# Kernel optimization log

Measured on AMD Instinct MI355X. Metric: run time of the kernel, lower is better.

Reference implementation:

```python
import jax, jax.numpy as jnp
import numpy as np

N, E, F_IN, F_E = 50000, 800000, 128, 16
R, H, C = 4, 4, 32            # num_relations, heads, out_channels
HC = H * C                     # 128
NEG_SLOPE = 0.2                # PyG RGATConv default negative_slope
EPS = 1e-16                    # PyG softmax epsilon


def rgat_conv(x, src, dst, edge_type, edge_attr, w, q, k, e, le, b, concat):
    """Faithful PyG RGATConv (additive-self-attention, across-relation, dim=1, aggr=add).
    x: [N,F]; w: [R,F,H*C]; q,k,e: [H*C,H]; le: [F_e,H*C]; b: bias."""
    n = x.shape[0]
    xw = jnp.einsum('nf,rfo->rno', x, w)              # [R,N,H*C] per-relation projections
    x_i = xw[edge_type, dst]                          # [E,H*C] target-node proj per edge
    x_j = xw[edge_type, src]                          # [E,H*C] source-node proj per edge
    qi = x_i @ q                                      # [E,H]
    kj = x_j @ k + (edge_attr @ le) @ e               # [E,H] (edge features folded into keys)
    alpha = jax.nn.leaky_relu(qi + kj, NEG_SLOPE)     # [E,H]
    # softmax over incoming edges of each destination node (across relations)
    amax = jax.ops.segment_max(alpha, dst, num_segments=n)
    ex = jnp.exp(alpha - amax[dst])
    denom = jax.ops.segment_sum(ex, dst, num_segments=n)
    alpha = ex / (denom[dst] + EPS)
    msg = alpha[:, :, None] * x_j.reshape(-1, H, C)   # [E,H,C]
    out = jax.ops.segment_sum(msg, dst, num_segments=n)  # [N,H,C] sum aggregation
    out = out.reshape(n, H * C) if concat else out.mean(axis=1)
    return out + b


def setup_inputs() -> dict:
    key = jax.random.key(0)
    ks = jax.random.split(key, 18)
    p = 0.05
    inp = {
        'x': jax.random.normal(ks[0], (N, F_IN), dtype=jnp.float32),
        'edge_index': jax.random.randint(ks[1], (2, E), 0, N, dtype=jnp.int64)
            if jax.config.jax_enable_x64 else jax.random.randint(ks[1], (2, E), 0, N).astype(jnp.int32),
        'edge_attr': jax.random.normal(ks[2], (E, F_E), dtype=jnp.float32),
        'edge_type': jax.random.randint(ks[3], (E,), 0, R).astype(jnp.int32),
        # conv1 params (in=F_IN, concat=True -> bias of size H*C)
        'w1': jax.random.normal(ks[4], (R, F_IN, HC), dtype=jnp.float32) * p,
        'q1': jax.random.normal(ks[5], (HC, H), dtype=jnp.float32) * p,
        'k1': jax.random.normal(ks[6], (HC, H), dtype=jnp.float32) * p,
        'e1': jax.random.normal(ks[7], (HC, H), dtype=jnp.float32) * p,
        'le1': jax.random.normal(ks[8], (F_E, HC), dtype=jnp.float32) * p,
        'b1': jnp.zeros((HC,), dtype=jnp.float32),
        # conv3 params (in=H*C=128, concat=False -> bias of size C)
        'w3': jax.random.normal(ks[9], (R, HC, HC), dtype=jnp.float32) * p,
        'q3': jax.random.normal(ks[10], (HC, H), dtype=jnp.float32) * p,
        'k3': jax.random.normal(ks[11], (HC, H), dtype=jnp.float32) * p,
        'e3': jax.random.normal(ks[12], (HC, H), dtype=jnp.float32) * p,
        'le3': jax.random.normal(ks[13], (F_E, HC), dtype=jnp.float32) * p,
        'b3': jnp.zeros((C,), dtype=jnp.float32),
    }
    return inp


def reference(x, edge_index, edge_attr, edge_type,
              w1, q1, k1, e1, le1, b1,
              w3, q3, k3, e3, le3, b3):
    src, dst = edge_index[0], edge_index[1]
    h = jax.nn.relu(rgat_conv(x, src, dst, edge_type, edge_attr,
                              w1, q1, k1, e1, le1, b1, concat=True))
    out = rgat_conv(h, src, dst, edge_type, edge_attr,
                    w3, q3, k3, e3, le3, b3, concat=False)
    return out
```

## Files before the change

kernel.cpp:

```cpp
#include <hip/hip_runtime.h>


#define NEG_SLOPE 0.2f
#define SOFT_EPS 1e-16f

typedef __attribute__((ext_vector_type(8))) short bf16x8;
typedef __attribute__((ext_vector_type(4))) float f32x4;
typedef __attribute__((ext_vector_type(4))) unsigned short u16x4;
typedef __attribute__((ext_vector_type(4))) _Float16 half4;
typedef __attribute__((ext_vector_type(8))) _Float16 half8;

__device__ __forceinline__ void bf16split(float f, unsigned short& h, unsigned short& l) {
  unsigned u = __float_as_uint(f);
  unsigned r = u + 0x7FFFu + ((u >> 16) & 1u);
  h = (unsigned short)(r >> 16);
  float fh = __uint_as_float(((unsigned)h) << 16);
  float d = f - fh;
  unsigned u2 = __float_as_uint(d);
  unsigned r2 = u2 + 0x7FFFu + ((u2 >> 16) & 1u);
  l = (unsigned short)(r2 >> 16);
}

__global__ void lee_kernel(const float* __restrict__ le1, const float* __restrict__ e1,
                           const float* __restrict__ le3, const float* __restrict__ e3,
                           float* __restrict__ lee) {
  int t = threadIdx.x;
  const float* le = (t < 64) ? le1 : le3;
  const float* ee = (t < 64) ? e1 : e3;
  int u = t & 63, f = u >> 2, h = u & 3;
  float acc = 0.f;
  for (int o = 0; o < 128; ++o) acc += le[f * 128 + o] * ee[o * 4 + h];
  lee[t] = acc;
}

__global__ __launch_bounds__(256) void wqk_kernel(
    const float* __restrict__ w1, const float* __restrict__ q1, const float* __restrict__ k1,
    const float* __restrict__ w3, const float* __restrict__ q3, const float* __restrict__ k3,
    float* __restrict__ wqk) {
  int idx = blockIdx.x * 256 + threadIdx.x;
  int L = idx >> 12, rem = idx & 4095;
  int r = rem >> 10, rem2 = rem & 1023, f = rem2 >> 3, j = rem2 & 7;
  const float* w = L ? w3 : w1;
  const float* qk = (j < 4) ? (L ? q3 : q1) : (L ? k3 : k1);
  int h = j & 3;
  const float* wrow = w + ((size_t)r * 128 + f) * 128;
  float acc = 0.f;
  for (int o = 0; o < 128; ++o) acc += wrow[o] * qk[o * 4 + h];
  wqk[idx] = acc;
}

__global__ __launch_bounds__(256) void hist_kernel(const int* __restrict__ dst,
                                                   int* __restrict__ deg, int E) {
  int e = blockIdx.x * 256 + threadIdx.x;
  if (e < E) atomicAdd(&deg[dst[e]], 1);
}

__global__ __launch_bounds__(256) void scanA_kernel(const int* __restrict__ deg,
                                                    int* __restrict__ bsum, int N) {
  int b = blockIdx.x, t = threadIdx.x;
  int base = b * 1024 + t * 4;
  int s = 0;
#pragma unroll
  for (int j = 0; j < 4; ++j) {
    int i = base + j;
    if (i < N) s += deg[i];
  }
#pragma unroll
  for (int o = 1; o < 64; o <<= 1) s += __shfl_xor(s, o);
  __shared__ int wsum[4];
  if ((t & 63) == 0) wsum[t >> 6] = s;
  __syncthreads();
  if (t == 0) bsum[b] = wsum[0] + wsum[1] + wsum[2] + wsum[3];
}

__global__ __launch_bounds__(256) void scanB_kernel(const int* __restrict__ bsum,
                                                    int* __restrict__ boff,
                                                    int* __restrict__ row_start,
                                                    int nb, int N) {
  int t = threadIdx.x;
  int v = (t < nb) ? bsum[t] : 0;
  int inc = v;
#pragma unroll
  for (int o = 1; o < 64; o <<= 1) {
    int u = __shfl_up(inc, o);
    if ((t & 63) >= o) inc += u;
  }
  __shared__ int wt[4];
  if ((t & 63) == 63) wt[t >> 6] = inc;
  __syncthreads();
  int add = 0;
  for (int wv = 0; wv < (t >> 6); ++wv) add += wt[wv];
  inc += add;
  if (t < nb) boff[t] = inc - v;
  if (t == 255) row_start[N] = inc;
}

__global__ __launch_bounds__(256) void scanC_kernel(const int* __restrict__ deg,
                                                    const int* __restrict__ boff,
                                                    int* __restrict__ row_start,
                                                    int* __restrict__ cursor, int N) {
  int b = blockIdx.x, t = threadIdx.x;
  int base = b * 1024 + t * 4;
  int d[4];
  int s = 0;
#pragma unroll
  for (int j = 0; j < 4; ++j) {
    int i = base + j;
    d[j] = (i < N) ? deg[i] : 0;
    s += d[j];
  }
  int inc = s;
#pragma unroll
  for (int o = 1; o < 64; o <<= 1) {
    int u = __shfl_up(inc, o);
    if ((t & 63) >= o) inc += u;
  }
  __shared__ int wt[4];
  if ((t & 63) == 63) wt[t >> 6] = inc;
  __syncthreads();
  int add = boff[b];
  for (int wv = 0; wv < (t >> 6); ++wv) add += wt[wv];
  int off = add + inc - s;
#pragma unroll
  for (int j = 0; j < 4; ++j) {
    int i = base + j;
    if (i < N) {
      row_start[i] = off;
      cursor[i] = off;
      off += d[j];
    }
  }
}

__global__ __launch_bounds__(256) void scatter_kernel(
    const int* __restrict__ src, const int* __restrict__ dst, const int* __restrict__ et,
    int* __restrict__ cursor, int4* __restrict__ es, int E) {
  int e = blockIdx.x * 256 + threadIdx.x;
  if (e >= E) return;
  int d = dst[e];
  int pos = atomicAdd(&cursor[d], 1);
  es[pos] = make_int4(src[e], d, et[e], e);
}

__global__ __launch_bounds__(256) void ek2_kernel(
    const int4* __restrict__ es, const float* __restrict__ ea,
    const float* __restrict__ lee, float* __restrict__ eks1,
    float* __restrict__ eks3, int E) {
  __shared__ float sl[128];
  if (threadIdx.x < 128) sl[threadIdx.x] = lee[threadIdx.x];
  __syncthreads();
  int i = blockIdx.x * 256 + threadIdx.x;
  if (i >= E) return;
  int eid = es[i].w;
  const float4* a4 = (const float4*)(ea + (size_t)eid * 16);
  float a1[4] = {0, 0, 0, 0}, a3[4] = {0, 0, 0, 0};
#pragma unroll
  for (int ii = 0; ii < 4; ++ii) {
    float4 v = a4[ii];
    int f = ii * 4;
#pragma unroll
    for (int h = 0; h < 4; ++h) {
      a1[h] += v.x * sl[f * 4 + h] + v.y * sl[(f + 1) * 4 + h] +
               v.z * sl[(f + 2) * 4 + h] + v.w * sl[(f + 3) * 4 + h];
      a3[h] += v.x * sl[64 + f * 4 + h] + v.y * sl[64 + (f + 1) * 4 + h] +
               v.z * sl[64 + (f + 2) * 4 + h] + v.w * sl[64 + (f + 3) * 4 + h];
    }
  }
  *(float4*)(eks1 + (size_t)i * 4) = make_float4(a1[0], a1[1], a1[2], a1[3]);
  *(float4*)(eks3 + (size_t)i * 4) = make_float4(a3[0], a3[1], a3[2], a3[3]);
}

__global__ __launch_bounds__(256) void convx_kernel(const float* __restrict__ in,
                                                    unsigned short* __restrict__ hi,
                                                    unsigned short* __restrict__ lo,
                                                    int total8) {
  int i = blockIdx.x * 256 + threadIdx.x;
  if (i >= total8) return;
  const float4* p = (const float4*)in + (size_t)i * 2;
  float4 a = p[0], b = p[1];
  float v[8] = {a.x, a.y, a.z, a.w, b.x, b.y, b.z, b.w};
  bf16x8 hv, lv;
#pragma unroll
  for (int j = 0; j < 8; ++j) {
    unsigned short h, l;
    bf16split(v[j], h, l);
    hv[j] = (short)h; lv[j] = (short)l;
  }
  *(bf16x8*)(hi + (size_t)i * 8) = hv;
  *(bf16x8*)(lo + (size_t)i * 8) = lv;
}

__global__ void convw_kernel(const float* __restrict__ w,
                             unsigned short* __restrict__ hiT,
                             unsigned short* __restrict__ loT) {
  int f = blockIdx.x, r = blockIdx.y, o = threadIdx.x;
  float v = w[((size_t)r * 128 + f) * 128 + o];
  unsigned short h, l;
  bf16split(v, h, l);
  hiT[((size_t)r * 128 + o) * 128 + f] = h;
  loT[((size_t)r * 128 + o) * 128 + f] = l;
}

__global__ __launch_bounds__(256) void proj_mfma_kernel(
    const unsigned short* __restrict__ xhi, const unsigned short* __restrict__ xlo,
    const unsigned short* __restrict__ whiT, const unsigned short* __restrict__ wloT,
    _Float16* __restrict__ xwh, int N) {
  __shared__ bf16x8 wl_h[2048];
  __shared__ bf16x8 wl_l[2048];
  int r = blockIdx.x;
  int nb = blockIdx.y * 128;
  int t = threadIdx.x;
  const unsigned short* wh = whiT + (size_t)r * (128 * 128);
  const unsigned short* wl = wloT + (size_t)r * (128 * 128);

#pragma unroll
  for (int j = 0; j < 8; ++j) {
    int i = j * 256 + t;
    int c = i & 15, q = (i >> 4) & 3, kc = (i >> 6) & 3, ot = i >> 8;
    int srco = (ot * 16 + c) * 128 + kc * 32 + q * 8;
    wl_h[i] = *(const bf16x8*)(wh + srco);
    wl_l[i] = *(const bf16x8*)(wl + srco);
  }
  __syncthreads();

  int wv = t >> 6;
  int lane = t & 63;
  int c = lane & 15, q = lane >> 4;
  int nodebase = nb + wv * 32;
  int n0 = nodebase + c;
  int n1 = nodebase + 16 + c;
  int n0c = n0 < N ? n0 : N - 1;
  int n1c = n1 < N ? n1 : N - 1;

  f32x4 acc[8][2];
#pragma unroll
  for (int ot = 0; ot < 8; ++ot)
#pragma unroll
    for (int nt = 0; nt < 2; ++nt) acc[ot][nt] = (f32x4){0.f, 0.f, 0.f, 0.f};

  bf16x8 xb[2][4];
  {
    int k0 = q * 8;
    xb[0][0] = *(const bf16x8*)(xhi + (size_t)n0c * 128 + k0);
    xb[0][1] = *(const bf16x8*)(xlo + (size_t)n0c * 128 + k0);
    xb[0][2] = *(const bf16x8*)(xhi + (size_t)n1c * 128 + k0);
    xb[0][3] = *(const bf16x8*)(xlo + (size_t)n1c * 128 + k0);
  }
#pragma unroll
  for (int kc = 0; kc < 4; ++kc) {
    if (kc < 3) {
      int k0 = (kc + 1) * 32 + q * 8;
      xb[(kc + 1) & 1][0] = *(const bf16x8*)(xhi + (size_t)n0c * 128 + k0);
      xb[(kc + 1) & 1][1] = *(const bf16x8*)(xlo + (size_t)n0c * 128 + k0);
      xb[(kc + 1) & 1][2] = *(const bf16x8*)(xhi + (size_t)n1c * 128 + k0);
      xb[(kc + 1) & 1][3] = *(const bf16x8*)(xlo + (size_t)n1c * 128 + k0);
    }
    bf16x8 b0h = xb[kc & 1][0], b0l = xb[kc & 1][1];
    bf16x8 b1h = xb[kc & 1][2], b1l = xb[kc & 1][3];
#pragma unroll
    for (int ot = 0; ot < 8; ++ot) {
      int fi = ((ot * 4 + kc) * 4 + q) * 16 + c;
      bf16x8 ah = wl_h[fi];
      bf16x8 al = wl_l[fi];
      acc[ot][0] = __builtin_amdgcn_mfma_f32_16x16x32_bf16(ah, b0h, acc[ot][0], 0, 0, 0);
      acc[ot][0] = __builtin_amdgcn_mfma_f32_16x16x32_bf16(ah, b0l, acc[ot][0], 0, 0, 0);
      acc[ot][0] = __builtin_amdgcn_mfma_f32_16x16x32_bf16(al, b0h, acc[ot][0], 0, 0, 0);
      acc[ot][1] = __builtin_amdgcn_mfma_f32_16x16x32_bf16(ah, b1h, acc[ot][1], 0, 0, 0);
      acc[ot][1] = __builtin_amdgcn_mfma_f32_16x16x32_bf16(ah, b1l, acc[ot][1], 0, 0, 0);
      acc[ot][1] = __builtin_amdgcn_mfma_f32_16x16x32_bf16(al, b1h, acc[ot][1], 0, 0, 0);
    }
  }

#pragma unroll
  for (int nt = 0; nt < 2; ++nt) {
    int n = nodebase + nt * 16 + c;
    if (n < N) {
      _Float16* basep = xwh + ((size_t)r * N + n) * 128 + q * 4;
#pragma unroll
      for (int ot = 0; ot < 8; ++ot) {
        f32x4 a = acc[ot][nt];
        half4 hv;
        hv[0] = (_Float16)a.x; hv[1] = (_Float16)a.y;
        hv[2] = (_Float16)a.z; hv[3] = (_Float16)a.w;
        *(half4*)(basep + ot * 16) = hv;
      }
    }
  }
}

__global__ __launch_bounds__(256) void qkx_kernel(
    const float* __restrict__ xin, const float* __restrict__ wqk,
    float* __restrict__ qn, float* __restrict__ kn, int N) {
  __shared__ float sx[64 * 132];
  __shared__ float swqk[4 * 1032];
  int nb = blockIdx.x * 64;
  int t = threadIdx.x;
#pragma unroll
  for (int j = 0; j < 16; ++j) {
    int i = j * 256 + t;
    swqk[(i >> 10) * 1032 + (i & 1023)] = wqk[i];
  }
#pragma unroll
  for (int j = 0; j < 8; ++j) {
    int i = j * 256 + t;
    int n = nb + (i >> 5); if (n >= N) n = N - 1;
    ((float4*)sx)[(i >> 5) * 33 + (i & 31)] =
        ((const float4*)(xin + (size_t)n * 128))[i & 31];
  }
  __syncthreads();
  int rl = t >> 2, r = t & 3;
  float aq0 = 0, aq1 = 0, aq2 = 0, aq3 = 0;
  float ak0 = 0, ak1 = 0, ak2 = 0, ak3 = 0;
  const float* xr = sx + rl * 132;
  const float* wb = swqk + r * 1032;
  for (int f = 0; f < 128; ++f) {
    float xv = xr[f];
    float4 qw = *(const float4*)(wb + f * 8);
    float4 kw = *(const float4*)(wb + f * 8 + 4);
    aq0 += xv * qw.x; aq1 += xv * qw.y; aq2 += xv * qw.z; aq3 += xv * qw.w;
    ak0 += xv * kw.x; ak1 += xv * kw.y; ak2 += xv * kw.z; ak3 += xv * kw.w;
  }
  int n = nb + rl;
  if (n < N) {
    *(float4*)(qn + ((size_t)r * N + n) * 4) = make_float4(aq0, aq1, aq2, aq3);
    *(float4*)(kn + ((size_t)r * N + n) * 4) = make_float4(ak0, ak1, ak2, ak3);
  }
}

__device__ __forceinline__ float4 edge_alpha(const int4* __restrict__ es,
                                             const float* __restrict__ qn,
                                             const float* __restrict__ kn,
                                             const float* __restrict__ eks,
                                             int i, int d, int N) {
  int4 v = es[i];
  float4 kv = *(const float4*)(kn + (v.z * N + v.x) * 4);
  float4 ev = ((const float4*)eks)[i];
  float4 q4 = *(const float4*)(qn + (v.z * N + d) * 4);
  float4 a = make_float4(q4.x + kv.x + ev.x, q4.y + kv.y + ev.y,
                         q4.z + kv.z + ev.z, q4.w + kv.w + ev.w);
  a.x = a.x > 0.f ? a.x : NEG_SLOPE * a.x;
  a.y = a.y > 0.f ? a.y : NEG_SLOPE * a.y;
  a.z = a.z > 0.f ? a.z : NEG_SLOPE * a.z;
  a.w = a.w > 0.f ? a.w : NEG_SLOPE * a.w;
  return a;
}

__global__ __launch_bounds__(256) void agg_kernel(
    const int4* __restrict__ es, const int* __restrict__ row_start,
    const float* __restrict__ qn, const float* __restrict__ kn,
    const float* __restrict__ eks, float* __restrict__ alpha_s,
    const _Float16* __restrict__ xwh, const float* __restrict__ bias,
    float* __restrict__ out, unsigned short* __restrict__ xhi,
    unsigned short* __restrict__ xlo, int N, int concat) {
  int d = blockIdx.x * 16 + (threadIdx.x >> 4);
  if (d >= N) return;
  int ql = threadIdx.x & 15;
  int rs = row_start[d], re = row_start[d + 1];
  int deg = re - rs;
  bool fast = (deg <= 64);

  float4 m = make_float4(-1e30f, -1e30f, -1e30f, -1e30f);
  float4 ar0 = m, ar1 = m, ar2 = m, ar3 = m;
  if (fast) {
#define SWEEPA(IT, AR)                                              \
    if (IT * 16 + ql < deg) {                                       \
      float4 a = edge_alpha(es, qn, kn, eks, rs + IT * 16 + ql, d, N); \
      AR = a;                                                       \
      m.x = fmaxf(m.x, a.x); m.y = fmaxf(m.y, a.y);                 \
      m.z = fmaxf(m.z, a.z); m.w = fmaxf(m.w, a.w);                 \
    }
    SWEEPA(0, ar0)
    SWEEPA(1, ar1)
    SWEEPA(2, ar2)
    SWEEPA(3, ar3)
#undef SWEEPA
  } else {
    for (int i = rs + ql; i < re; i += 16) {
      float4 a = edge_alpha(es, qn, kn, eks, i, d, N);
      ((float4*)alpha_s)[i] = a;
      m.x = fmaxf(m.x, a.x); m.y = fmaxf(m.y, a.y);
      m.z = fmaxf(m.z, a.z); m.w = fmaxf(m.w, a.w);
    }
  }
#pragma unroll
  for (int o = 1; o < 16; o <<= 1) {
    m.x = fmaxf(m.x, __shfl_xor(m.x, o));
    m.y = fmaxf(m.y, __shfl_xor(m.y, o));
    m.z = fmaxf(m.z, __shfl_xor(m.z, o));
    m.w = fmaxf(m.w, __shfl_xor(m.w, o));
  }

  float4 s = make_float4(0.f, 0.f, 0.f, 0.f);
  if (fast) {
#define SWEEPB(IT, AR)                                                       \
    if (IT * 16 + ql < deg) {                                                \
      float4 e4 = make_float4(__expf(AR.x - m.x), __expf(AR.y - m.y),        \
                              __expf(AR.z - m.z), __expf(AR.w - m.w));       \
      ((float4*)alpha_s)[rs + IT * 16 + ql] = e4;                            \
      s.x += e4.x; s.y += e4.y; s.z += e4.z; s.w += e4.w;                    \
    }
    SWEEPB(0, ar0)
    SWEEPB(1, ar1)
    SWEEPB(2, ar2)
    SWEEPB(3, ar3)
#undef SWEEPB
  } else {
    for (int i = rs + ql; i < re; i += 16) {
      float4 a = ((const float4*)alpha_s)[i];
      float4 e4 = make_float4(__expf(a.x - m.x), __expf(a.y - m.y),
                              __expf(a.z - m.z), __expf(a.w - m.w));
      ((float4*)alpha_s)[i] = e4;
      s.x += e4.x; s.y += e4.y; s.z += e4.z; s.w += e4.w;
    }
  }
#pragma unroll
  for (int o = 1; o < 16; o <<= 1) {
    s.x += __shfl_xor(s.x, o); s.y += __shfl_xor(s.y, o);
    s.z += __shfl_xor(s.z, o); s.w += __shfl_xor(s.w, o);
  }

  int h = ql >> 2;
  float smh = (h == 0) ? s.x : (h == 1) ? s.y : (h == 2) ? s.z : s.w;
  float rden = 1.f / (smh + SOFT_EPS);

  float acc[8];
#pragma unroll
  for (int j = 0; j < 8; ++j) acc[j] = 0.f;
  int e = rs;
  for (; e + 2 <= re; e += 2) {
    int4 a0 = es[e];
    int4 a1 = es[e + 1];
    float w0 = alpha_s[e * 4 + h];
    float w1 = alpha_s[(e + 1) * 4 + h];
    half8 x0 = *(const half8*)(xwh + (a0.z * N + a0.x) * 128 + ql * 8);
    half8 x1 = *(const half8*)(xwh + (a1.z * N + a1.x) * 128 + ql * 8);
#pragma unroll
    for (int j = 0; j < 8; ++j) {
      acc[j] = fmaf((float)x0[j], w0, acc[j]);
      acc[j] = fmaf((float)x1[j], w1, acc[j]);
    }
  }
  if (e < re) {
    int4 a0 = es[e];
    float w0 = alpha_s[e * 4 + h];
    half8 x0 = *(const half8*)(xwh + (a0.z * N + a0.x) * 128 + ql * 8);
#pragma unroll
    for (int j = 0; j < 8; ++j) acc[j] = fmaf((float)x0[j], w0, acc[j]);
  }
#pragma unroll
  for (int j = 0; j < 8; ++j) acc[j] *= rden;

  if (concat) {
    float4 b0 = ((const float4*)bias)[ql * 2];
    float4 b1 = ((const float4*)bias)[ql * 2 + 1];
    float v[8] = {acc[0] + b0.x, acc[1] + b0.y, acc[2] + b0.z, acc[3] + b0.w,
                  acc[4] + b1.x, acc[5] + b1.y, acc[6] + b1.z, acc[7] + b1.w};
    u16x4 hv0, lv0, hv1, lv1;
#pragma unroll
    for (int j = 0; j < 8; ++j) {
      v[j] = v[j] > 0.f ? v[j] : 0.f;
      unsigned short hh, ll;
      bf16split(v[j], hh, ll);
      if (j < 4) { hv0[j] = hh; lv0[j] = ll; }
      else { hv1[j - 4] = hh; lv1[j - 4] = ll; }
    }
    float* orow = out + (size_t)d * 128 + ql * 8;
    *(float4*)orow = make_float4(v[0], v[1], v[2], v[3]);
    *(float4*)(orow + 4) = make_float4(v[4], v[5], v[6], v[7]);
    *(u16x4*)(xhi + (size_t)d * 128 + ql * 8) = hv0;
    *(u16x4*)(xhi + (size_t)d * 128 + ql * 8 + 4) = hv1;
    *(u16x4*)(xlo + (size_t)d * 128 + ql * 8) = lv0;
    *(u16x4*)(xlo + (size_t)d * 128 + ql * 8 + 4) = lv1;
  } else {
#pragma unroll
    for (int j = 0; j < 8; ++j) {
      acc[j] += __shfl_xor(acc[j], 4);
      acc[j] += __shfl_xor(acc[j], 8);
    }
    if (ql < 4) {
      float4 b0 = ((const float4*)bias)[ql * 2];
      float4 b1 = ((const float4*)bias)[ql * 2 + 1];
      float* orow = out + (size_t)d * 32 + ql * 8;
      *(float4*)orow = make_float4(0.25f * acc[0] + b0.x, 0.25f * acc[1] + b0.y,
                                   0.25f * acc[2] + b0.z, 0.25f * acc[3] + b0.w);
      *(float4*)(orow + 4) = make_float4(0.25f * acc[4] + b1.x, 0.25f * acc[5] + b1.y,
                                         0.25f * acc[6] + b1.z, 0.25f * acc[7] + b1.w);
    }
  }
}

extern "C" void kernel_launch(void* const* d_in, const int* in_sizes, int n_in,
                              void* d_out, int out_size, void* d_ws, size_t ws_size,
                              hipStream_t stream) {
  const float* x   = (const float*)d_in[0];
  const int*   ei  = (const int*)d_in[1];
  const float* ea  = (const float*)d_in[2];
  const int*   etp = (const int*)d_in[3];
  const float* w1  = (const float*)d_in[4];
  const float* q1  = (const float*)d_in[5];
  const float* k1  = (const float*)d_in[6];
  const float* e1  = (const float*)d_in[7];
  const float* le1 = (const float*)d_in[8];
  const float* b1  = (const float*)d_in[9];
  const float* w3  = (const float*)d_in[10];
  const float* q3  = (const float*)d_in[11];
  const float* k3  = (const float*)d_in[12];
  const float* e3  = (const float*)d_in[13];
  const float* le3 = (const float*)d_in[14];
  const float* b3  = (const float*)d_in[15];
  const int N = in_sizes[0] / 128;
  const int E = in_sizes[3];
  const int* srcp = ei;
  const int* dstp = ei + E;

  float* ws   = (float*)d_ws;
  _Float16* xwh = (_Float16*)ws;
  float* qn   = ws + (size_t)2 * N * 128;
  float* kn   = qn + (size_t)4 * N * 4;
  float* eks1 = kn + (size_t)4 * N * 4;
  float* eks3 = eks1 + (size_t)E * 4;
  float* alph = eks3 + (size_t)E * 4;
  float* hbuf = alph + (size_t)E * 4;
  float* leeb = hbuf + (size_t)N * 128;
  float* wqkb = leeb + 128;
  int* deg      = (int*)(wqkb + 8192);
  int* rowst    = deg + N;
  int* cursor   = rowst + N + 1;
  int* bsum     = cursor + N;
  int* boff     = bsum + 256;
  uintptr_t pe = (uintptr_t)(boff + 256);
  pe = (pe + 15) & ~(uintptr_t)15;
  int4* es      = (int4*)pe;
  uintptr_t pa = (uintptr_t)(es + E);
  pa = (pa + 255) & ~(uintptr_t)255;
  unsigned short* xhi  = (unsigned short*)pa;
  unsigned short* xlo  = xhi + (size_t)N * 128;
  unsigned short* whiT = xlo + (size_t)N * 128;
  unsigned short* wloT = whiT + 4 * 128 * 128;
  (void)ws_size; (void)n_in; (void)out_size;

  int eb   = (E + 255) / 256;
  int nb16 = (N + 15) / 16;
  int nbs  = (N + 1023) / 1024;
  int pgy  = (N + 127) / 128;
  int qxb  = (N + 63) / 64;
  int cxb  = (N * 128 / 8 + 255) / 256;

  hipMemsetAsync(deg, 0, (size_t)N * sizeof(int), stream);
  hist_kernel<<<eb, 256, 0, stream>>>(dstp, deg, E);
  scanA_kernel<<<nbs, 256, 0, stream>>>(deg, bsum, N);
  scanB_kernel<<<1, 256, 0, stream>>>(bsum, boff, rowst, nbs, N);
  scanC_kernel<<<nbs, 256, 0, stream>>>(deg, boff, rowst, cursor, N);
  scatter_kernel<<<eb, 256, 0, stream>>>(srcp, dstp, etp, cursor, es, E);
  lee_kernel<<<1, 128, 0, stream>>>(le1, e1, le3, e3, leeb);
  ek2_kernel<<<eb, 256, 0, stream>>>(es, ea, leeb, eks1, eks3, E);
  wqk_kernel<<<32, 256, 0, stream>>>(w1, q1, k1, w3, q3, k3, wqkb);
  convx_kernel<<<cxb, 256, 0, stream>>>(x, xhi, xlo, N * 128 / 8);

  for (int layer = 0; layer < 2; ++layer) {
    const float* xin = layer ? hbuf : x;
    const float* w   = layer ? w3 : w1;
    const float* eks = layer ? eks3 : eks1;
    const float* bias = layer ? b3 : b1;
    float* outp = layer ? (float*)d_out : hbuf;

    convw_kernel<<<dim3(128, 4), 128, 0, stream>>>(w, whiT, wloT);
    proj_mfma_kernel<<<dim3(4, pgy), 256, 0, stream>>>(xhi, xlo, whiT, wloT, xwh, N);
    qkx_kernel<<<qxb, 256, 0, stream>>>(xin, wqkb + layer * 4096, qn, kn, N);
    agg_kernel<<<nb16, 256, 0, stream>>>(es, rowst, qn, kn, eks, xwh == 0 ? alph : alph, xwh,
                                         bias, outp, xhi, xlo, N, layer == 0 ? 1 : 0);
  }
}
```

Baseline: 496.5 us.

## Merge independent preprocessing and projection kernels into heterogeneous multi-role launches

Independent stages now share launches, with block-index ranges picking the role: histogram with x conversion, both layers' weight conversion, wqk and lee; scatter with the qk projection; edge-key computation with the layer-1 MFMA projection; and the layer-2 projection with its qk projection. Weight conversion for both layers happens once up front into separate buffers. The aggregation kernel is also restructured, with a fast path that keeps per-edge alphas in registers for low-degree nodes and a gather loop unrolled by four. This cuts launch count and lets bandwidth-bound and compute-bound stages overlap, at the cost of larger dynamic shared memory per block and mixed-role blocks.

```diff
diff --git a/kernel.cpp b/kernel.cpp
--- a/kernel.cpp
+++ b/kernel.cpp
@@ -21,10 +21,73 @@
   l = (unsigned short)(r2 >> 16);
 }
 
-__global__ void lee_kernel(const float* __restrict__ le1, const float* __restrict__ e1,
-                           const float* __restrict__ le3, const float* __restrict__ e3,
-                           float* __restrict__ lee) {
+
+__device__ __forceinline__ void hist_body(int id, const int* __restrict__ dst,
+                                          int* __restrict__ deg, int E) {
+  int e = id * 256 + (int)threadIdx.x;
+  if (e < E) atomicAdd(&deg[dst[e]], 1);
+}
+
+__device__ __forceinline__ void convx_body(int id, const float* __restrict__ in,
+                                           unsigned short* __restrict__ hi,
+                                           unsigned short* __restrict__ lo, int total8) {
+  int i = id * 256 + (int)threadIdx.x;
+  if (i >= total8) return;
+  const float4* p = (const float4*)in + (size_t)i * 2;
+  float4 a = p[0], b = p[1];
+  float v[8] = {a.x, a.y, a.z, a.w, b.x, b.y, b.z, b.w};
+  bf16x8 hv, lv;
+#pragma unroll
+  for (int j = 0; j < 8; ++j) {
+    unsigned short h, l;
+    bf16split(v[j], h, l);
+    hv[j] = (short)h; lv[j] = (short)l;
+  }
+  *(bf16x8*)(hi + (size_t)i * 8) = hv;
+  *(bf16x8*)(lo + (size_t)i * 8) = lv;
+}
+
+__device__ __forceinline__ void convw_body(int idx, const float* __restrict__ w1,
+                                           const float* __restrict__ w3,
+                                           unsigned short* __restrict__ whiT1,
+                                           unsigned short* __restrict__ wloT1,
+                                           unsigned short* __restrict__ whiT3,
+                                           unsigned short* __restrict__ wloT3) {
+  if (idx >= 131072) return;
+  int L = idx >> 16;
+  int rem = idx & 65535;
+  int r = rem >> 14, rem2 = rem & 16383, f = rem2 >> 7, o = rem2 & 127;
+  const float* w = L ? w3 : w1;
+  unsigned short* hiT = L ? whiT3 : whiT1;
+  unsigned short* loT = L ? wloT3 : wloT1;
+  float v = w[(r * 128 + f) * 128 + o];
+  unsigned short h, l;
+  bf16split(v, h, l);
+  hiT[(r * 128 + o) * 128 + f] = h;
+  loT[(r * 128 + o) * 128 + f] = l;
+}
+
+__device__ __forceinline__ void wqk_body(int idx, const float* __restrict__ w1,
+                                         const float* __restrict__ q1, const float* __restrict__ k1,
+                                         const float* __restrict__ w3, const float* __restrict__ q3,
+                                         const float* __restrict__ k3, float* __restrict__ wqk) {
+  if (idx >= 8192) return;
+  int L = idx >> 12, rem = idx & 4095;
+  int r = rem >> 10, rem2 = rem & 1023, f = rem2 >> 3, j = rem2 & 7;
+  const float* w = L ? w3 : w1;
+  const float* qk = (j < 4) ? (L ? q3 : q1) : (L ? k3 : k1);
+  int h = j & 3;
+  const float* wrow = w + (r * 128 + f) * 128;
+  float acc = 0.f;
+  for (int o = 0; o < 128; ++o) acc += wrow[o] * qk[o * 4 + h];
+  wqk[idx] = acc;
+}
+
+__device__ __forceinline__ void lee_body(const float* __restrict__ le1, const float* __restrict__ e1,
+                                         const float* __restrict__ le3, const float* __restrict__ e3,
+                                         float* __restrict__ lee) {
   int t = threadIdx.x;
+  if (t >= 128) return;
   const float* le = (t < 64) ? le1 : le3;
   const float* ee = (t < 64) ? e1 : e3;
   int u = t & 63, f = u >> 2, h = u & 3;
@@ -33,27 +96,38 @@
   lee[t] = acc;
 }
 
-__global__ __launch_bounds__(256) void wqk_kernel(
+__global__ __launch_bounds__(256) void pre_kernel(
+    const int* __restrict__ dst, int* __restrict__ deg, int E,
+    const float* __restrict__ x, unsigned short* __restrict__ xhi,
+    unsigned short* __restrict__ xlo, int total8,
     const float* __restrict__ w1, const float* __restrict__ q1, const float* __restrict__ k1,
     const float* __restrict__ w3, const float* __restrict__ q3, const float* __restrict__ k3,
-    float* __restrict__ wqk) {
-  int idx = blockIdx.x * 256 + threadIdx.x;
-  int L = idx >> 12, rem = idx & 4095;
-  int r = rem >> 10, rem2 = rem & 1023, f = rem2 >> 3, j = rem2 & 7;
-  const float* w = L ? w3 : w1;
-  const float* qk = (j < 4) ? (L ? q3 : q1) : (L ? k3 : k1);
-  int h = j & 3;
-  const float* wrow = w + ((size_t)r * 128 + f) * 128;
-  float acc = 0.f;
-  for (int o = 0; o < 128; ++o) acc += wrow[o] * qk[o * 4 + h];
-  wqk[idx] = acc;
-}
-
-__global__ __launch_bounds__(256) void hist_kernel(const int* __restrict__ dst,
-                                                   int* __restrict__ deg, int E) {
-  int e = blockIdx.x * 256 + threadIdx.x;
-  if (e < E) atomicAdd(&deg[dst[e]], 1);
-}
+    float* __restrict__ wqk,
+    const float* __restrict__ le1, const float* __restrict__ e1,
+    const float* __restrict__ le3, const float* __restrict__ e3, float* __restrict__ lee,
+    unsigned short* __restrict__ whiT1, unsigned short* __restrict__ wloT1,
+    unsigned short* __restrict__ whiT3, unsigned short* __restrict__ wloT3,
+    int nAB, int eb, int cxb) {
+  int bid = blockIdx.x;
+  if (bid < nAB) {
+    int id = bid >> 1;
+    if (bid & 1) {
+      if (id < eb) hist_body(id, dst, deg, E);
+    } else {
+      if (id < cxb) convx_body(id, x, xhi, xlo, total8);
+    }
+  } else {
+    int b2 = bid - nAB;
+    if (b2 < 512) {
+      convw_body(b2 * 256 + (int)threadIdx.x, w1, w3, whiT1, wloT1, whiT3, wloT3);
+    } else if (b2 < 544) {
+      wqk_body((b2 - 512) * 256 + (int)threadIdx.x, w1, q1, k1, w3, q3, k3, wqk);
+    } else {
+      lee_body(le1, e1, le3, e3, lee);
+    }
+  }
+}
+
 
 __global__ __launch_bounds__(256) void scanA_kernel(const int* __restrict__ deg,
                                                     int* __restrict__ bsum, int N) {
@@ -132,168 +206,25 @@
   }
 }
 
-__global__ __launch_bounds__(256) void scatter_kernel(
-    const int* __restrict__ src, const int* __restrict__ dst, const int* __restrict__ et,
-    int* __restrict__ cursor, int4* __restrict__ es, int E) {
-  int e = blockIdx.x * 256 + threadIdx.x;
+
+__device__ __forceinline__ void scatter_body(int id, const int* __restrict__ src,
+                                             const int* __restrict__ dst,
+                                             const int* __restrict__ et,
+                                             int* __restrict__ cursor,
+                                             int4* __restrict__ es, int E) {
+  int e = id * 256 + (int)threadIdx.x;
   if (e >= E) return;
   int d = dst[e];
   int pos = atomicAdd(&cursor[d], 1);
   es[pos] = make_int4(src[e], d, et[e], e);
 }
 
-__global__ __launch_bounds__(256) void ek2_kernel(
-    const int4* __restrict__ es, const float* __restrict__ ea,
-    const float* __restrict__ lee, float* __restrict__ eks1,
-    float* __restrict__ eks3, int E) {
-  __shared__ float sl[128];
-  if (threadIdx.x < 128) sl[threadIdx.x] = lee[threadIdx.x];
-  __syncthreads();
-  int i = blockIdx.x * 256 + threadIdx.x;
-  if (i >= E) return;
-  int eid = es[i].w;
-  const float4* a4 = (const float4*)(ea + (size_t)eid * 16);
-  float a1[4] = {0, 0, 0, 0}, a3[4] = {0, 0, 0, 0};
-#pragma unroll
-  for (int ii = 0; ii < 4; ++ii) {
-    float4 v = a4[ii];
-    int f = ii * 4;
-#pragma unroll
-    for (int h = 0; h < 4; ++h) {
-      a1[h] += v.x * sl[f * 4 + h] + v.y * sl[(f + 1) * 4 + h] +
-               v.z * sl[(f + 2) * 4 + h] + v.w * sl[(f + 3) * 4 + h];
-      a3[h] += v.x * sl[64 + f * 4 + h] + v.y * sl[64 + (f + 1) * 4 + h] +
-               v.z * sl[64 + (f + 2) * 4 + h] + v.w * sl[64 + (f + 3) * 4 + h];
-    }
-  }
-  *(float4*)(eks1 + (size_t)i * 4) = make_float4(a1[0], a1[1], a1[2], a1[3]);
-  *(float4*)(eks3 + (size_t)i * 4) = make_float4(a3[0], a3[1], a3[2], a3[3]);
-}
-
-__global__ __launch_bounds__(256) void convx_kernel(const float* __restrict__ in,
-                                                    unsigned short* __restrict__ hi,
-                                                    unsigned short* __restrict__ lo,
-                                                    int total8) {
-  int i = blockIdx.x * 256 + threadIdx.x;
-  if (i >= total8) return;
-  const float4* p = (const float4*)in + (size_t)i * 2;
-  float4 a = p[0], b = p[1];
-  float v[8] = {a.x, a.y, a.z, a.w, b.x, b.y, b.z, b.w};
-  bf16x8 hv, lv;
-#pragma unroll
-  for (int j = 0; j < 8; ++j) {
-    unsigned short h, l;
-    bf16split(v[j], h, l);
-    hv[j] = (short)h; lv[j] = (short)l;
-  }
-  *(bf16x8*)(hi + (size_t)i * 8) = hv;
-  *(bf16x8*)(lo + (size_t)i * 8) = lv;
-}
-
-__global__ void convw_kernel(const float* __restrict__ w,
-                             unsigned short* __restrict__ hiT,
-                             unsigned short* __restrict__ loT) {
-  int f = blockIdx.x, r = blockIdx.y, o = threadIdx.x;
-  float v = w[((size_t)r * 128 + f) * 128 + o];
-  unsigned short h, l;
-  bf16split(v, h, l);
-  hiT[((size_t)r * 128 + o) * 128 + f] = h;
-  loT[((size_t)r * 128 + o) * 128 + f] = l;
-}
-
-__global__ __launch_bounds__(256) void proj_mfma_kernel(
-    const unsigned short* __restrict__ xhi, const unsigned short* __restrict__ xlo,
-    const unsigned short* __restrict__ whiT, const unsigned short* __restrict__ wloT,
-    _Float16* __restrict__ xwh, int N) {
-  __shared__ bf16x8 wl_h[2048];
-  __shared__ bf16x8 wl_l[2048];
-  int r = blockIdx.x;
-  int nb = blockIdx.y * 128;
-  int t = threadIdx.x;
-  const unsigned short* wh = whiT + (size_t)r * (128 * 128);
-  const unsigned short* wl = wloT + (size_t)r * (128 * 128);
-
-#pragma unroll
-  for (int j = 0; j < 8; ++j) {
-    int i = j * 256 + t;
-    int c = i & 15, q = (i >> 4) & 3, kc = (i >> 6) & 3, ot = i >> 8;
-    int srco = (ot * 16 + c) * 128 + kc * 32 + q * 8;
-    wl_h[i] = *(const bf16x8*)(wh + srco);
-    wl_l[i] = *(const bf16x8*)(wl + srco);
-  }
-  __syncthreads();
-
-  int wv = t >> 6;
-  int lane = t & 63;
-  int c = lane & 15, q = lane >> 4;
-  int nodebase = nb + wv * 32;
-  int n0 = nodebase + c;
-  int n1 = nodebase + 16 + c;
-  int n0c = n0 < N ? n0 : N - 1;
-  int n1c = n1 < N ? n1 : N - 1;
-
-  f32x4 acc[8][2];
-#pragma unroll
-  for (int ot = 0; ot < 8; ++ot)
-#pragma unroll
-    for (int nt = 0; nt < 2; ++nt) acc[ot][nt] = (f32x4){0.f, 0.f, 0.f, 0.f};
-
-  bf16x8 xb[2][4];
-  {
-    int k0 = q * 8;
-    xb[0][0] = *(const bf16x8*)(xhi + (size_t)n0c * 128 + k0);
-    xb[0][1] = *(const bf16x8*)(xlo + (size_t)n0c * 128 + k0);
-    xb[0][2] = *(const bf16x8*)(xhi + (size_t)n1c * 128 + k0);
-    xb[0][3] = *(const bf16x8*)(xlo + (size_t)n1c * 128 + k0);
-  }
-#pragma unroll
-  for (int kc = 0; kc < 4; ++kc) {
-    if (kc < 3) {
-      int k0 = (kc + 1) * 32 + q * 8;
-      xb[(kc + 1) & 1][0] = *(const bf16x8*)(xhi + (size_t)n0c * 128 + k0);
-      xb[(kc + 1) & 1][1] = *(const bf16x8*)(xlo + (size_t)n0c * 128 + k0);
-      xb[(kc + 1) & 1][2] = *(const bf16x8*)(xhi + (size_t)n1c * 128 + k0);
-      xb[(kc + 1) & 1][3] = *(const bf16x8*)(xlo + (size_t)n1c * 128 + k0);
-    }
-    bf16x8 b0h = xb[kc & 1][0], b0l = xb[kc & 1][1];
-    bf16x8 b1h = xb[kc & 1][2], b1l = xb[kc & 1][3];
-#pragma unroll
-    for (int ot = 0; ot < 8; ++ot) {
-      int fi = ((ot * 4 + kc) * 4 + q) * 16 + c;
-      bf16x8 ah = wl_h[fi];
-      bf16x8 al = wl_l[fi];
-      acc[ot][0] = __builtin_amdgcn_mfma_f32_16x16x32_bf16(ah, b0h, acc[ot][0], 0, 0, 0);
-      acc[ot][0] = __builtin_amdgcn_mfma_f32_16x16x32_bf16(ah, b0l, acc[ot][0], 0, 0, 0);
-      acc[ot][0] = __builtin_amdgcn_mfma_f32_16x16x32_bf16(al, b0h, acc[ot][0], 0, 0, 0);
-      acc[ot][1] = __builtin_amdgcn_mfma_f32_16x16x32_bf16(ah, b1h, acc[ot][1], 0, 0, 0);
-      acc[ot][1] = __builtin_amdgcn_mfma_f32_16x16x32_bf16(ah, b1l, acc[ot][1], 0, 0, 0);
-      acc[ot][1] = __builtin_amdgcn_mfma_f32_16x16x32_bf16(al, b1h, acc[ot][1], 0, 0, 0);
-    }
-  }
-
-#pragma unroll
-  for (int nt = 0; nt < 2; ++nt) {
-    int n = nodebase + nt * 16 + c;
-    if (n < N) {
-      _Float16* basep = xwh + ((size_t)r * N + n) * 128 + q * 4;
-#pragma unroll
-      for (int ot = 0; ot < 8; ++ot) {
-        f32x4 a = acc[ot][nt];
-        half4 hv;
-        hv[0] = (_Float16)a.x; hv[1] = (_Float16)a.y;
-        hv[2] = (_Float16)a.z; hv[3] = (_Float16)a.w;
-        *(half4*)(basep + ot * 16) = hv;
-      }
-    }
-  }
-}
-
-__global__ __launch_bounds__(256) void qkx_kernel(
-    const float* __restrict__ xin, const float* __restrict__ wqk,
-    float* __restrict__ qn, float* __restrict__ kn, int N) {
-  __shared__ float sx[64 * 132];
-  __shared__ float swqk[4 * 1032];
-  int nb = blockIdx.x * 64;
+__device__ __forceinline__ void qkx_body(int nbid, char* smem, const float* __restrict__ xin,
+                                         const float* __restrict__ wqk, float* __restrict__ qn,
+                                         float* __restrict__ kn, int N) {
+  float* sx = (float*)smem;
+  float* swqk = sx + 64 * 132;
+  int nb = nbid * 64;
   int t = threadIdx.x;
 #pragma unroll
   for (int j = 0; j < 16; ++j) {
@@ -326,6 +257,174 @@
     *(float4*)(kn + ((size_t)r * N + n) * 4) = make_float4(ak0, ak1, ak2, ak3);
   }
 }
+
+__global__ __launch_bounds__(256) void sc_kernel(
+    const int* __restrict__ src, const int* __restrict__ dst, const int* __restrict__ et,
+    int* __restrict__ cursor, int4* __restrict__ es, int E,
+    const float* __restrict__ xin, const float* __restrict__ wqk,
+    float* __restrict__ qn, float* __restrict__ kn, int N, int qxb) {
+  extern __shared__ char smem[];
+  int bid = blockIdx.x;
+  int g = bid / 5, r5 = bid - g * 5;
+  if (r5 == 4) {
+    if (g < qxb) qkx_body(g, smem, xin, wqk, qn, kn, N);
+  } else {
+    scatter_body(g * 4 + r5, src, dst, et, cursor, es, E);
+  }
+}
+
+
+__device__ __forceinline__ void ek2_body(int id, char* smem, const int4* __restrict__ es,
+                                         const float* __restrict__ ea,
+                                         const float* __restrict__ lee,
+                                         float* __restrict__ eks1, float* __restrict__ eks3,
+                                         int E) {
+  float* sl = (float*)smem;
+  if (threadIdx.x < 128) sl[threadIdx.x] = lee[threadIdx.x];
+  __syncthreads();
+  int i = id * 256 + (int)threadIdx.x;
+  if (i >= E) return;
+  int eid = es[i].w;
+  const float4* a4 = (const float4*)(ea + (size_t)eid * 16);
+  float a1[4] = {0, 0, 0, 0}, a3[4] = {0, 0, 0, 0};
+#pragma unroll
+  for (int ii = 0; ii < 4; ++ii) {
+    float4 v = a4[ii];
+    int f = ii * 4;
+#pragma unroll
+    for (int h = 0; h < 4; ++h) {
+      a1[h] += v.x * sl[f * 4 + h] + v.y * sl[(f + 1) * 4 + h] +
+               v.z * sl[(f + 2) * 4 + h] + v.w * sl[(f + 3) * 4 + h];
+      a3[h] += v.x * sl[64 + f * 4 + h] + v.y * sl[64 + (f + 1) * 4 + h] +
+               v.z * sl[64 + (f + 2) * 4 + h] + v.w * sl[64 + (f + 3) * 4 + h];
+    }
+  }
+  *(float4*)(eks1 + (size_t)i * 4) = make_float4(a1[0], a1[1], a1[2], a1[3]);
+  *(float4*)(eks3 + (size_t)i * 4) = make_float4(a3[0], a3[1], a3[2], a3[3]);
+}
+
+__device__ __forceinline__ void proj_body(int pid, char* smem,
+                                          const unsigned short* __restrict__ xhi,
+                                          const unsigned short* __restrict__ xlo,
+                                          const unsigned short* __restrict__ whiT,
+                                          const unsigned short* __restrict__ wloT,
+                                          _Float16* __restrict__ xwh, int N) {
+  bf16x8* wl_h = (bf16x8*)smem;
+  bf16x8* wl_l = wl_h + 2048;
+  int r = pid & 3;
+  int nb = (pid >> 2) * 128;
+  int t = threadIdx.x;
+  const unsigned short* wh = whiT + r * (128 * 128);
+  const unsigned short* wl = wloT + r * (128 * 128);
+
+#pragma unroll
+  for (int j = 0; j < 8; ++j) {
+    int i = j * 256 + t;
+    int c = i & 15, q = (i >> 4) & 3, kc = (i >> 6) & 3, ot = i >> 8;
+    int srco = (ot * 16 + c) * 128 + kc * 32 + q * 8;
+    wl_h[i] = *(const bf16x8*)(wh + srco);
+    wl_l[i] = *(const bf16x8*)(wl + srco);
+  }
+  __syncthreads();
+
+  int wv = t >> 6;
+  int lane = t & 63;
+  int c = lane & 15, q = lane >> 4;
+  int nodebase = nb + wv * 32;
+  int n0 = nodebase + c;
+  int n1 = nodebase + 16 + c;
+  int n0c = n0 < N ? n0 : N - 1;
+  int n1c = n1 < N ? n1 : N - 1;
+
+  f32x4 acc[8][2];
+#pragma unroll
+  for (int ot = 0; ot < 8; ++ot)
+#pragma unroll
+    for (int nt = 0; nt < 2; ++nt) acc[ot][nt] = (f32x4){0.f, 0.f, 0.f, 0.f};
+
+  bf16x8 xb[2][4];
+  {
+    int k0 = q * 8;
+    xb[0][0] = *(const bf16x8*)(xhi + (size_t)n0c * 128 + k0);
+    xb[0][1] = *(const bf16x8*)(xlo + (size_t)n0c * 128 + k0);
+    xb[0][2] = *(const bf16x8*)(xhi + (size_t)n1c * 128 + k0);
+    xb[0][3] = *(const bf16x8*)(xlo + (size_t)n1c * 128 + k0);
+  }
+#pragma unroll
+  for (int kc = 0; kc < 4; ++kc) {
+    if (kc < 3) {
+      int k0 = (kc + 1) * 32 + q * 8;
+      xb[(kc + 1) & 1][0] = *(const bf16x8*)(xhi + (size_t)n0c * 128 + k0);
+      xb[(kc + 1) & 1][1] = *(const bf16x8*)(xlo + (size_t)n0c * 128 + k0);
+      xb[(kc + 1) & 1][2] = *(const bf16x8*)(xhi + (size_t)n1c * 128 + k0);
+      xb[(kc + 1) & 1][3] = *(const bf16x8*)(xlo + (size_t)n1c * 128 + k0);
+    }
+    bf16x8 b0h = xb[kc & 1][0], b0l = xb[kc & 1][1];
+    bf16x8 b1h = xb[kc & 1][2], b1l = xb[kc & 1][3];
+#pragma unroll
+    for (int ot = 0; ot < 8; ++ot) {
+      int fi = ((ot * 4 + kc) * 4 + q) * 16 + c;
+      bf16x8 ah = wl_h[fi];
+      bf16x8 al = wl_l[fi];
+      acc[ot][0] = __builtin_amdgcn_mfma_f32_16x16x32_bf16(ah, b0h, acc[ot][0], 0, 0, 0);
+      acc[ot][0] = __builtin_amdgcn_mfma_f32_16x16x32_bf16(ah, b0l, acc[ot][0], 0, 0, 0);
+      acc[ot][0] = __builtin_amdgcn_mfma_f32_16x16x32_bf16(al, b0h, acc[ot][0], 0, 0, 0);
+      acc[ot][1] = __builtin_amdgcn_mfma_f32_16x16x32_bf16(ah, b1h, acc[ot][1], 0, 0, 0);
+      acc[ot][1] = __builtin_amdgcn_mfma_f32_16x16x32_bf16(ah, b1l, acc[ot][1], 0, 0, 0);
+      acc[ot][1] = __builtin_amdgcn_mfma_f32_16x16x32_bf16(al, b1h, acc[ot][1], 0, 0, 0);
+    }
+  }
+
+#pragma unroll
+  for (int nt = 0; nt < 2; ++nt) {
+    int n = nodebase + nt * 16 + c;
+    if (n < N) {
+      _Float16* basep = xwh + ((size_t)r * N + n) * 128 + q * 4;
+#pragma unroll
+      for (int ot = 0; ot < 8; ++ot) {
+        f32x4 a = acc[ot][nt];
+        half4 hv;
+        hv[0] = (_Float16)a.x; hv[1] = (_Float16)a.y;
+        hv[2] = (_Float16)a.z; hv[3] = (_Float16)a.w;
+        *(half4*)(basep + ot * 16) = hv;
+      }
+    }
+  }
+}
+
+__global__ __launch_bounds__(256) void ep1_kernel(
+    const int4* __restrict__ es, const float* __restrict__ ea, const float* __restrict__ lee,
+    float* __restrict__ eks1, float* __restrict__ eks3, int E,
+    const unsigned short* __restrict__ xhi, const unsigned short* __restrict__ xlo,
+    const unsigned short* __restrict__ whiT, const unsigned short* __restrict__ wloT,
+    _Float16* __restrict__ xwh, int N, int pjb) {
+  extern __shared__ char smem[];
+  int bid = blockIdx.x;
+  int g = bid / 3, r3 = bid - g * 3;
+  if (r3 == 2) {
+    if (g < pjb) proj_body(g, smem, xhi, xlo, whiT, wloT, xwh, N);
+  } else {
+    ek2_body(g * 2 + r3, smem, es, ea, lee, eks1, eks3, E);
+  }
+}
+
+__global__ __launch_bounds__(256) void p2_kernel(
+    const unsigned short* __restrict__ xhi, const unsigned short* __restrict__ xlo,
+    const unsigned short* __restrict__ whiT, const unsigned short* __restrict__ wloT,
+    _Float16* __restrict__ xwh, int N,
+    const float* __restrict__ xin, const float* __restrict__ wqk,
+    float* __restrict__ qn, float* __restrict__ kn, int pjb, int qxb) {
+  extern __shared__ char smem[];
+  int bid = blockIdx.x;
+  int g = bid / 3, r3 = bid - g * 3;
+  if (r3 == 2) {
+    if (g < qxb) qkx_body(g, smem, xin, wqk, qn, kn, N);
+  } else {
+    int id = g * 2 + r3;
+    if (id < pjb) proj_body(id, smem, xhi, xlo, whiT, wloT, xwh, N);
+  }
+}
+
 
 __device__ __forceinline__ float4 edge_alpha(const int4* __restrict__ es,
                                              const float* __restrict__ qn,
@@ -345,6 +444,10 @@
   return a;
 }
 
+__device__ __forceinline__ float4 max4(float4 a, float4 b) {
+  return make_float4(fmaxf(a.x, b.x), fmaxf(a.y, b.y), fmaxf(a.z, b.z), fmaxf(a.w, b.w));
+}
+
 __global__ __launch_bounds__(256) void agg_kernel(
     const int4* __restrict__ es, const int* __restrict__ row_start,
     const float* __restrict__ qn, const float* __restrict__ kn,
@@ -357,95 +460,107 @@
   int ql = threadIdx.x & 15;
   int rs = row_start[d], re = row_start[d + 1];
   int deg = re - rs;
-  bool fast = (deg <= 64);
-
-  float4 m = make_float4(-1e30f, -1e30f, -1e30f, -1e30f);
-  float4 ar0 = m, ar1 = m, ar2 = m, ar3 = m;
-  if (fast) {
-#define SWEEPA(IT, AR)                                              \
-    if (IT * 16 + ql < deg) {                                       \
-      float4 a = edge_alpha(es, qn, kn, eks, rs + IT * 16 + ql, d, N); \
-      AR = a;                                                       \
-      m.x = fmaxf(m.x, a.x); m.y = fmaxf(m.y, a.y);                 \
-      m.z = fmaxf(m.z, a.z); m.w = fmaxf(m.w, a.w);                 \
-    }
-    SWEEPA(0, ar0)
-    SWEEPA(1, ar1)
-    SWEEPA(2, ar2)
-    SWEEPA(3, ar3)
-#undef SWEEPA
-  } else {
-    for (int i = rs + ql; i < re; i += 16) {
-      float4 a = edge_alpha(es, qn, kn, eks, i, d, N);
-      ((float4*)alpha_s)[i] = a;
-      m.x = fmaxf(m.x, a.x); m.y = fmaxf(m.y, a.y);
-      m.z = fmaxf(m.z, a.z); m.w = fmaxf(m.w, a.w);
-    }
-  }
-#pragma unroll
-  for (int o = 1; o < 16; o <<= 1) {
-    m.x = fmaxf(m.x, __shfl_xor(m.x, o));
-    m.y = fmaxf(m.y, __shfl_xor(m.y, o));
-    m.z = fmaxf(m.z, __shfl_xor(m.z, o));
-    m.w = fmaxf(m.w, __shfl_xor(m.w, o));
-  }
-
-  float4 s = make_float4(0.f, 0.f, 0.f, 0.f);
-  if (fast) {
-#define SWEEPB(IT, AR)                                                       \
-    if (IT * 16 + ql < deg) {                                                \
-      float4 e4 = make_float4(__expf(AR.x - m.x), __expf(AR.y - m.y),        \
-                              __expf(AR.z - m.z), __expf(AR.w - m.w));       \
-      ((float4*)alpha_s)[rs + IT * 16 + ql] = e4;                            \
-      s.x += e4.x; s.y += e4.y; s.z += e4.z; s.w += e4.w;                    \
-    }
-    SWEEPB(0, ar0)
-    SWEEPB(1, ar1)
-    SWEEPB(2, ar2)
-    SWEEPB(3, ar3)
+  int h = ql >> 2;
+
+  float acc[8];
+#pragma unroll
+  for (int j = 0; j < 8; ++j) acc[j] = 0.f;
+  float rden = 0.f;
+
+  if (deg > 0) {
+    float4 m = make_float4(-1e30f, -1e30f, -1e30f, -1e30f);
+    float4 ar0 = m, ar1 = m, ar2 = m, ar3 = m;
+    bool fast = (deg <= 64);
+    bool v0 = ql < deg, v1 = 16 + ql < deg, v2 = 32 + ql < deg, v3 = 48 + ql < deg;
+    if (fast) {
+      int dm1 = deg - 1;
+      int o0 = v0 ? ql : dm1;
+      int o1 = v1 ? 16 + ql : dm1;
+      int o2 = v2 ? 32 + ql : dm1;
+      int o3 = v3 ? 48 + ql : dm1;
+      float4 a0 = edge_alpha(es, qn, kn, eks, rs + o0, d, N);
+      float4 a1 = edge_alpha(es, qn, kn, eks, rs + o1, d, N);
+      float4 a2 = edge_alpha(es, qn, kn, eks, rs + o2, d, N);
+      float4 a3 = edge_alpha(es, qn, kn, eks, rs + o3, d, N);
+      if (v0) { ar0 = a0; m = max4(m, a0); }
+      if (v1) { ar1 = a1; m = max4(m, a1); }
+      if (v2) { ar2 = a2; m = max4(m, a2); }
+      if (v3) { ar3 = a3; m = max4(m, a3); }
+    } else {
+      for (int i = rs + ql; i < re; i += 16) {
+        float4 a = edge_alpha(es, qn, kn, eks, i, d, N);
+        ((float4*)alpha_s)[i] = a;
+        m = max4(m, a);
+      }
+    }
+#pragma unroll
+    for (int o = 1; o < 16; o <<= 1) {
+      m.x = fmaxf(m.x, __shfl_xor(m.x, o));
+      m.y = fmaxf(m.y, __shfl_xor(m.y, o));
+      m.z = fmaxf(m.z, __shfl_xor(m.z, o));
+      m.w = fmaxf(m.w, __shfl_xor(m.w, o));
+    }
+
+    float4 s = make_float4(0.f, 0.f, 0.f, 0.f);
+    if (fast) {
+#define SWEEPB(V, AR, OFF)                                                   \
+      if (V) {                                                               \
+        float4 e4 = make_float4(__expf(AR.x - m.x), __expf(AR.y - m.y),      \
+                                __expf(AR.z - m.z), __expf(AR.w - m.w));     \
+        ((float4*)alpha_s)[rs + OFF + ql] = e4;                              \
+        s.x += e4.x; s.y += e4.y; s.z += e4.z; s.w += e4.w;                  \
+      }
+      SWEEPB(v0, ar0, 0)
+      SWEEPB(v1, ar1, 16)
+      SWEEPB(v2, ar2, 32)
+      SWEEPB(v3, ar3, 48)
 #undef SWEEPB
-  } else {
-    for (int i = rs + ql; i < re; i += 16) {
-      float4 a = ((const float4*)alpha_s)[i];
-      float4 e4 = make_float4(__expf(a.x - m.x), __expf(a.y - m.y),
-                              __expf(a.z - m.z), __expf(a.w - m.w));
-      ((float4*)alpha_s)[i] = e4;
-      s.x += e4.x; s.y += e4.y; s.z += e4.z; s.w += e4.w;
-    }
-  }
-#pragma unroll
-  for (int o = 1; o < 16; o <<= 1) {
-    s.x += __shfl_xor(s.x, o); s.y += __shfl_xor(s.y, o);
-    s.z += __shfl_xor(s.z, o); s.w += __shfl_xor(s.w, o);
-  }
-
-  int h = ql >> 2;
-  float smh = (h == 0) ? s.x : (h == 1) ? s.y : (h == 2) ? s.z : s.w;
-  float rden = 1.f / (smh + SOFT_EPS);
-
-  float acc[8];
-#pragma unroll
-  for (int j = 0; j < 8; ++j) acc[j] = 0.f;
-  int e = rs;
-  for (; e + 2 <= re; e += 2) {
-    int4 a0 = es[e];
-    int4 a1 = es[e + 1];
-    float w0 = alpha_s[e * 4 + h];
-    float w1 = alpha_s[(e + 1) * 4 + h];
-    half8 x0 = *(const half8*)(xwh + (a0.z * N + a0.x) * 128 + ql * 8);
-    half8 x1 = *(const half8*)(xwh + (a1.z * N + a1.x) * 128 + ql * 8);
-#pragma unroll
-    for (int j = 0; j < 8; ++j) {
-      acc[j] = fmaf((float)x0[j], w0, acc[j]);
-      acc[j] = fmaf((float)x1[j], w1, acc[j]);
-    }
-  }
-  if (e < re) {
-    int4 a0 = es[e];
-    float w0 = alpha_s[e * 4 + h];
-    half8 x0 = *(const half8*)(xwh + (a0.z * N + a0.x) * 128 + ql * 8);
-#pragma unroll
-    for (int j = 0; j < 8; ++j) acc[j] = fmaf((float)x0[j], w0, acc[j]);
+    } else {
+      for (int i = rs + ql; i < re; i += 16) {
+        float4 a = ((const float4*)alpha_s)[i];
+        float4 e4 = make_float4(__expf(a.x - m.x), __expf(a.y - m.y),
+                                __expf(a.z - m.z), __expf(a.w - m.w));
+        ((float4*)alpha_s)[i] = e4;
+        s.x += e4.x; s.y += e4.y; s.z += e4.z; s.w += e4.w;
+      }
+    }
+#pragma unroll
+    for (int o = 1; o < 16; o <<= 1) {
+      s.x += __shfl_xor(s.x, o); s.y += __shfl_xor(s.y, o);
+      s.z += __shfl_xor(s.z, o); s.w += __shfl_xor(s.w, o);
+    }
+    float smh = (h == 0) ? s.x : (h == 1) ? s.y : (h == 2) ? s.z : s.w;
+    rden = 1.f / (smh + SOFT_EPS);
+
+    int e = rs;
+    for (; e + 4 <= re; e += 4) {
+      int4 a0 = es[e];
+      int4 a1 = es[e + 1];
+      int4 a2 = es[e + 2];
+      int4 a3 = es[e + 3];
+      float w0 = alpha_s[e * 4 + h];
+      float w1 = alpha_s[(e + 1) * 4 + h];
+      float w2 = alpha_s[(e + 2) * 4 + h];
+      float w3 = alpha_s[(e + 3) * 4 + h];
+      half8 x0 = *(const half8*)(xwh + (a0.z * N + a0.x) * 128 + ql * 8);
+      half8 x1 = *(const half8*)(xwh + (a1.z * N + a1.x) * 128 + ql * 8);
+      half8 x2 = *(const half8*)(xwh + (a2.z * N + a2.x) * 128 + ql * 8);
+      half8 x3 = *(const half8*)(xwh + (a3.z * N + a3.x) * 128 + ql * 8);
+#pragma unroll
+      for (int j = 0; j < 8; ++j) {
+        acc[j] = fmaf((float)x0[j], w0, acc[j]);
+        acc[j] = fmaf((float)x1[j], w1, acc[j]);
+        acc[j] = fmaf((float)x2[j], w2, acc[j]);
+        acc[j] = fmaf((float)x3[j], w3, acc[j]);
+      }
+    }
+    for (; e < re; ++e) {
+      int4 a0 = es[e];
+      float w0 = alpha_s[e * 4 + h];
+      half8 x0 = *(const half8*)(xwh + (a0.z * N + a0.x) * 128 + ql * 8);
+#pragma unroll
+      for (int j = 0; j < 8; ++j) acc[j] = fmaf((float)x0[j], w0, acc[j]);
+    }
   }
 #pragma unroll
   for (int j = 0; j < 8; ++j) acc[j] *= rden;
@@ -533,41 +648,53 @@
   int4* es      = (int4*)pe;
   uintptr_t pa = (uintptr_t)(es + E);
   pa = (pa + 255) & ~(uintptr_t)255;
-  unsigned short* xhi  = (unsigned short*)pa;
-  unsigned short* xlo  = xhi + (size_t)N * 128;
-  unsigned short* whiT = xlo + (size_t)N * 128;
-  unsigned short* wloT = whiT + 4 * 128 * 128;
+  unsigned short* xhi   = (unsigned short*)pa;
+  unsigned short* xlo   = xhi + (size_t)N * 128;
+  unsigned short* whiT1 = xlo + (size_t)N * 128;
+  unsigned short* wloT1 = whiT1 + 4 * 128 * 128;
+  unsigned short* whiT3 = wloT1 + 4 * 128 * 128;
+  unsigned short* wloT3 = whiT3 + 4 * 128 * 128;
   (void)ws_size; (void)n_in; (void)out_size;
 
   int eb   = (E + 255) / 256;
   int nb16 = (N + 15) / 16;
   int nbs  = (N + 1023) / 1024;
   int pgy  = (N + 127) / 128;
+  int pjb  = 4 * pgy;
   int qxb  = (N + 63) / 64;
   int cxb  = (N * 128 / 8 + 255) / 256;
 
   hipMemsetAsync(deg, 0, (size_t)N * sizeof(int), stream);
-  hist_kernel<<<eb, 256, 0, stream>>>(dstp, deg, E);
+
+  int M = eb > cxb ? eb : cxb;
+  int nAB = 2 * M;
+  int preg = nAB + 512 + 32 + 1;
+  pre_kernel<<<preg, 256, 0, stream>>>(dstp, deg, E, x, xhi, xlo, N * 128 / 8,
+                                       w1, q1, k1, w3, q3, k3, wqkb,
+                                       le1, e1, le3, e3, leeb,
+                                       whiT1, wloT1, whiT3, wloT3, nAB, eb, cxb);
   scanA_kernel<<<nbs, 256, 0, stream>>>(deg, bsum, N);
   scanB_kernel<<<1, 256, 0, stream>>>(bsum, boff, rowst, nbs, N);
   scanC_kernel<<<nbs, 256, 0, stream>>>(deg, boff, rowst, cursor, N);
-  scatter_kernel<<<eb, 256, 0, stream>>>(srcp, dstp, etp, cursor, es, E);
-  lee_kernel<<<1, 128, 0, stream>>>(le1, e1, le3, e3, leeb);
-  ek2_kernel<<<eb, 256, 0, stream>>>(es, ea, leeb, eks1, eks3, E);
-  wqk_kernel<<<32, 256, 0, stream>>>(w1, q1, k1, w3, q3, k3, wqkb);
-  convx_kernel<<<cxb, 256, 0, stream>>>(x, xhi, xlo, N * 128 / 8);
-
-  for (int layer = 0; layer < 2; ++layer) {
-    const float* xin = layer ? hbuf : x;
-    const float* w   = layer ? w3 : w1;
-    const float* eks = layer ? eks3 : eks1;
-    const float* bias = layer ? b3 : b1;
-    float* outp = layer ? (float*)d_out : hbuf;
-
-    convw_kernel<<<dim3(128, 4), 128, 0, stream>>>(w, whiT, wloT);
-    proj_mfma_kernel<<<dim3(4, pgy), 256, 0, stream>>>(xhi, xlo, whiT, wloT, xwh, N);
-    qkx_kernel<<<qxb, 256, 0, stream>>>(xin, wqkb + layer * 4096, qn, kn, N);
-    agg_kernel<<<nb16, 256, 0, stream>>>(es, rowst, qn, kn, eks, xwh == 0 ? alph : alph, xwh,
-                                         bias, outp, xhi, xlo, N, layer == 0 ? 1 : 0);
-  }
-}
+
+  int scq = (eb + 3) / 4;
+  int scg = 5 * (scq > qxb ? scq : qxb);
+  sc_kernel<<<scg, 256, 50304, stream>>>(srcp, dstp, etp, cursor, es, E,
+                                         x, wqkb, qn, kn, N, qxb);
+
+  int ekh = (eb + 1) / 2;
+  int e1g = 3 * (ekh > pjb ? ekh : pjb);
+  ep1_kernel<<<e1g, 256, 65536, stream>>>(es, ea, leeb, eks1, eks3, E,
+                                          xhi, xlo, whiT1, wloT1, xwh, N, pjb);
+
+  agg_kernel<<<nb16, 256, 0, stream>>>(es, rowst, qn, kn, eks1, alph, xwh,
+                                       b1, hbuf, xhi, xlo, N, 1);
+
+  int pjh = (pjb + 1) / 2;
+  int p2g = 3 * (pjh > qxb ? pjh : qxb);
+  p2_kernel<<<p2g, 256, 65536, stream>>>(xhi, xlo, whiT3, wloT3, xwh, N,
+                                         hbuf, wqkb + 4096, qn, kn, pjb, qxb);
+
+  agg_kernel<<<nb16, 256, 0, stream>>>(es, rowst, qn, kn, eks3, alph, xwh,
+                                       b3, (float*)d_out, xhi, xlo, N, 0);
+}
```

New measurement: 441.0 us. 1.13x faster.
